# Optimization experiments

Measured on AMD Instinct MI355X. Metric: run time of the kernel, lower is better.

The kernel has to match this reference:

```python
import jax, jax.numpy as jnp
import numpy as np

EPS = 1e-6  # torch F.pairwise_distance default eps (added to diff before norm)


def setup_inputs() -> dict:
    key = jax.random.key(0)
    k1, k2 = jax.random.split(key)
    B, D, n = 4096, 1024, 64
    K = n * n
    x = jax.random.normal(k1, (B, D), dtype=jnp.float32)
    weight = jax.random.normal(k2, (D, K), dtype=jnp.float32)  # SOM codebook
    # locations = [(gx, gy) for gx in range(n) for gy in range(n)]
    gx, gy = jnp.meshgrid(jnp.arange(n), jnp.arange(n), indexing='ij')
    locations = jnp.stack([gx, gy], axis=-1).reshape(K, 2).astype(jnp.float32)
    return {"x": x, "weight": weight, "locations": locations}


def _pairwise_l2(x, weight):
    # torch: norm(x[:, :, None] - weight[None] + EPS, p=2, dim=1) -> [B, K]
    # Expanded algebraically to avoid the [B, D, K] intermediate:
    D = x.shape[1]
    x2 = jnp.sum(x * x, axis=1, keepdims=True)            # [B, 1]
    w2 = jnp.sum(weight * weight, axis=0, keepdims=True)  # [1, K]
    xw = x @ weight                                        # [B, K] GEMM
    sx = jnp.sum(x, axis=1, keepdims=True)                 # [B, 1]
    sw = jnp.sum(weight, axis=0, keepdims=True)            # [1, K]
    d2 = x2 - 2.0 * xw + w2 + 2.0 * EPS * (sx - sw) + D * EPS * EPS
    return jnp.sqrt(jnp.maximum(d2, 0.0))


def reference(x, weight, locations):
    B = x.shape[0]
    dists = _pairwise_l2(x, weight)                        # [B, K]
    losses = jnp.min(dists, axis=1, keepdims=True)         # [B, 1]
    bmu_indexes = jnp.argmin(dists, axis=1, keepdims=True)  # [B, 1] int
    bmu_locations = locations[bmu_indexes]                 # [B, 1, 2]
    loss = jnp.sum(losses) / B                             # scalar
    return bmu_locations, loss, bmu_indexes
```

## Files before the change

kernel.cpp:

```cpp
#include <hip/hip_runtime.h>

#define EPS 1e-6f

constexpr int Bn = 4096;
constexpr int Dn = 1024;
constexpr int Kn = 4096;

typedef __attribute__((ext_vector_type(4))) float f32x4;
typedef __attribute__((ext_vector_type(2))) long long ll2;

__device__ inline int pk_fp8_lo(float a, float b, int old) {
    return __builtin_amdgcn_cvt_pk_fp8_f32(a, b, old, false);
}
__device__ inline int pk_fp8_hi(float a, float b, int old) {
    return __builtin_amdgcn_cvt_pk_fp8_f32(a, b, old, true);
}

__device__ inline float packcand(float s, int k) {
    unsigned b = __float_as_uint(fmaxf(s, 0.5f));
    return __uint_as_float((b & 0xFFFFF000u) | (unsigned)k);
}

__global__ __launch_bounds__(256) void som_prep(
    const float* __restrict__ x, const float* __restrict__ w,
    unsigned char* __restrict__ xf8, float* __restrict__ rrow,
    float* __restrict__ wtf, unsigned char* __restrict__ wf8,
    float* __restrict__ cpart) {
    __shared__ float t[64][65];
    __shared__ float cp[4][64];
    __shared__ float red[8];
    const int tid = threadIdx.x;
    const int bid = blockIdx.x;
    if (bid < 2048) {
        const int lane = tid & 63, wid = tid >> 6;
        size_t i = (size_t)bid * 256 + tid;
        const float4* p = (const float4*)x;
        float4 a = p[i * 2], b = p[i * 2 + 1];
        int lo = pk_fp8_lo(a.x, a.y, 0); lo = pk_fp8_hi(a.z, a.w, lo);
        int hi = pk_fp8_lo(b.x, b.y, 0); hi = pk_fp8_hi(b.z, b.w, hi);
        ((int2*)xf8)[i] = make_int2(lo, hi);
        float s2 = a.x*a.x + a.y*a.y + a.z*a.z + a.w*a.w
                 + b.x*b.x + b.y*b.y + b.z*b.z + b.w*b.w;
        float s1 = a.x + a.y + a.z + a.w + b.x + b.y + b.z + b.w;
        #pragma unroll
        for (int off = 1; off < 64; off <<= 1) {
            s2 += __shfl_xor(s2, off);
            s1 += __shfl_xor(s1, off);
        }
        if (lane == 0) { red[wid] = s2; red[4 + wid] = s1; }
        __syncthreads();
        if (tid == 0)
            rrow[bid * 2] = (red[0] + red[1])
                + 2.f * EPS * (red[4] + red[5]) + (float)Dn * EPS * EPS;
        if (tid == 128)
            rrow[bid * 2 + 1] = (red[2] + red[3])
                + 2.f * EPS * (red[6] + red[7]) + (float)Dn * EPS * EPS;
    } else {
        const int tb = bid - 2048;
        const int kb = tb & 63, db = tb >> 6;
        const int k0 = kb * 64, d0 = db * 64;
        const int tx = tid & 63, ty = tid >> 6;
        #pragma unroll
        for (int i = 0; i < 16; ++i) {
            int d = i * 4 + ty;
            t[d][tx] = w[(size_t)(d0 + d) * Kn + k0 + tx];
        }
        __syncthreads();
        #pragma unroll
        for (int i = 0; i < 16; ++i) {
            int kr = i * 4 + ty;
            float v = t[tx][kr];
            wtf[(size_t)(k0 + kr) * Dn + d0 + tx] = v;
            wf8[(size_t)(k0 + kr) * Dn + d0 + tx] =
                (unsigned char)(pk_fp8_lo(v, v, 0) & 0xFF);
        }
        float cs = 0.f;
        #pragma unroll
        for (int j = 0; j < 16; ++j) {
            float v = t[ty * 16 + j][tx];
            cs = fmaf(v, v - 2.f * EPS, cs);
        }
        cp[ty][tx] = cs;
        __syncthreads();
        if (ty == 0)
            cpart[(size_t)db * Kn + k0 + tx] = cp[0][tx] + cp[1][tx] + cp[2][tx] + cp[3][tx];
    }
}

__global__ __launch_bounds__(256, 3) void som_gemm_fp8(
    const unsigned char* __restrict__ xf8, const unsigned char* __restrict__ wf8,
    const float* __restrict__ cpart, float* __restrict__ pval) {
    __shared__ __align__(16) unsigned char As[128 * 144];
    __shared__ __align__(16) unsigned char Bs[128 * 144];
    const int tid = threadIdx.x;
    const int lane = tid & 63;
    const int wid = tid >> 6;
    const int wm = wid >> 1, wn = wid & 1;
    const int f = blockIdx.x;
    const int xcd = f & 7;
    const int ib = f >> 3;
    const int rb = xcd * 4 + (ib & 3);
    const int cb = ib >> 2;
    const int rowBase = rb * 128, colBase = cb * 128;

    int offA[4];
    const unsigned char* gsrcA[4];
    const unsigned char* gsrcB[4];
    #pragma unroll
    for (int i = 0; i < 4; ++i) {
        int g = i * 256 + tid;
        int r = g >> 3, s = g & 7;
        offA[i] = r * 144 + (2 * (s & 1)) * 32 + (s >> 1) * 8;
        gsrcA[i] = xf8 + (size_t)(rowBase + r) * Dn + s * 16;
        gsrcB[i] = wf8 + (size_t)(colBase + r) * Dn + s * 16;
    }

    f32x4 acc[4][4] = {};
    ll2 ra[4], rbv[4];
    #pragma unroll
    for (int i = 0; i < 4; ++i) {
        ra[i]  = *(const ll2*)(gsrcA[i]);
        rbv[i] = *(const ll2*)(gsrcB[i]);
    }

    const int mrA = (wm * 64 + (lane & 15)) * 144;
    const int nrB = (wn * 64 + (lane & 15)) * 144;
    const int qoff = (lane >> 4) * 32;

    for (int it = 0; it < 8; ++it) {
        #pragma unroll
        for (int i = 0; i < 4; ++i) {
            *(long long*)&As[offA[i]]      = ra[i][0];
            *(long long*)&As[offA[i] + 32] = ra[i][1];
            *(long long*)&Bs[offA[i]]      = rbv[i][0];
            *(long long*)&Bs[offA[i] + 32] = rbv[i][1];
        }
        __syncthreads();
        if (it < 7) {
            int d0 = (it + 1) * 128;
            #pragma unroll
            for (int i = 0; i < 4; ++i) {
                ra[i]  = *(const ll2*)(gsrcA[i] + d0);
                rbv[i] = *(const ll2*)(gsrcB[i] + d0);
            }
        }
        #pragma unroll
        for (int kk2 = 0; kk2 < 2; ++kk2) {
            ll2 a2[4], b2[4];
            #pragma unroll
            for (int i = 0; i < 4; ++i) {
                a2[i] = *(const ll2*)&As[mrA + i * 16 * 144 + qoff + kk2 * 16];
                b2[i] = *(const ll2*)&Bs[nrB + i * 16 * 144 + qoff + kk2 * 16];
            }
            #pragma unroll
            for (int i = 0; i < 4; ++i)
                #pragma unroll
                for (int j = 0; j < 4; ++j) {
                    acc[i][j] = __builtin_amdgcn_mfma_f32_16x16x32_fp8_fp8(
                        a2[i][0], b2[j][0], acc[i][j], 0, 0, 0);
                    acc[i][j] = __builtin_amdgcn_mfma_f32_16x16x32_fp8_fp8(
                        a2[i][1], b2[j][1], acc[i][j], 0, 0, 0);
                }
        }
        __syncthreads();
    }

    const int cn = lane & 15, q = lane >> 4;
    const int nbase = colBase + wn * 64;
    float cv[4];
    #pragma unroll
    for (int j = 0; j < 4; ++j) {
        float s = 0.f;
        #pragma unroll
        for (int db = 0; db < 16; ++db)
            s += cpart[(size_t)db * Kn + nbase + j * 16 + cn];
        cv[j] = s;
    }
    #pragma unroll
    for (int i = 0; i < 4; ++i) {
        #pragma unroll
        for (int rg = 0; rg < 4; ++rg) {
            float p1 = 3.4e38f, p2 = 3.4e38f;
            #pragma unroll
            for (int j = 0; j < 4; ++j) {
                float p = packcand(fmaf(-2.f, acc[i][j][rg], cv[j]),
                                   nbase + j * 16 + cn);
                float lo = fminf(p1, p), hi = fmaxf(p1, p);
                p1 = lo; p2 = fminf(p2, hi);
            }
            #pragma unroll
            for (int off = 1; off < 16; off <<= 1) {
                float o1 = __shfl_xor(p1, off);
                float o2 = __shfl_xor(p2, off);
                float lo = fminf(p1, o1), hi = fmaxf(p1, o1);
                p1 = lo; p2 = fminf(hi, fminf(p2, o2));
            }
            if (cn == 0) {
                int mrow = rowBase + wm * 64 + i * 16 + q * 4 + rg;
                size_t e = (size_t)mrow * 128 + cb * 4 + wn * 2;
                pval[e] = p1; pval[e + 1] = p2;
            }
        }
    }
}

__global__ __launch_bounds__(256) void som_finalize(
    const float* __restrict__ x, const float* __restrict__ wtf,
    const float* __restrict__ cpart, const float* __restrict__ loc,
    const float* __restrict__ pval, const float* __restrict__ rrow,
    float* __restrict__ dist, float* __restrict__ out) {
    const int lane = threadIdx.x & 63;
    const int row = blockIdx.x * 4 + (threadIdx.x >> 6);

    const float4* xr = (const float4*)(x + (size_t)row * Dn);
    float4 xv[4];
    #pragma unroll
    for (int j = 0; j < 4; ++j) xv[j] = xr[lane * 4 + j];
    const float rrv = rrow[row];

    float v0 = pval[(size_t)row * 128 + lane];
    float v1 = pval[(size_t)row * 128 + 64 + lane];
    float g = fminf(v0, v1);
    #pragma unroll
    for (int off = 1; off < 64; off <<= 1) g = fminf(g, __shfl_xor(g, off));
    const float thr = g + 30.0f;
    unsigned long long m0 = __ballot(v0 <= thr);
    unsigned long long m1 = __ballot(v1 <= thr);

    float bestd2 = 3.4e38f; int bestk = 0x7fffffff;
    #pragma unroll
    for (int slot = 0; slot < 2; ++slot) {
        unsigned long long m = slot ? m1 : m0;
        float vs = slot ? v1 : v0;
        while (m) {
            int src = __builtin_ctzll(m); m &= m - 1;
            int k = ((int)__float_as_uint(__shfl(vs, src))) & 0xFFF;
            const float4* wr = (const float4*)(wtf + (size_t)k * Dn);
            float dt = 0.f;
            #pragma unroll
            for (int j = 0; j < 4; ++j) {
                float4 wv = wr[lane * 4 + j];
                dt += xv[j].x * wv.x + xv[j].y * wv.y + xv[j].z * wv.z + xv[j].w * wv.w;
            }
            #pragma unroll
            for (int off = 1; off < 64; off <<= 1) dt += __shfl_xor(dt, off);
            float ck = 0.f;
            #pragma unroll
            for (int db = 0; db < 16; ++db) ck += cpart[(size_t)db * Kn + k];
            float d2 = rrv + ck - 2.f * dt;
            if (d2 < bestd2 || (d2 == bestd2 && k < bestk)) { bestd2 = d2; bestk = k; }
        }
    }
    if (lane == 0) {
        out[2 * row]     = loc[2 * bestk];
        out[2 * row + 1] = loc[2 * bestk + 1];
        out[8193 + row]  = (float)bestk;
        dist[row]        = sqrtf(fmaxf(bestd2, 0.f));
    }
}

__global__ __launch_bounds__(256) void som_loss(const float* __restrict__ dist,
                                                float* __restrict__ out) {
    __shared__ float red[4];
    const int tid = threadIdx.x;
    const int lane = tid & 63, wid = tid >> 6;
    const float4* p = (const float4*)dist;
    float s = 0.f;
    #pragma unroll
    for (int j = 0; j < 4; ++j) {
        float4 v = p[tid + j * 256];
        s += v.x + v.y + v.z + v.w;
    }
    #pragma unroll
    for (int off = 1; off < 64; off <<= 1) s += __shfl_xor(s, off);
    if (lane == 0) red[wid] = s;
    __syncthreads();
    if (tid == 0)
        out[8192] = (red[0] + red[1] + red[2] + red[3]) * (1.0f / (float)Bn);
}

extern "C" void kernel_launch(void* const* d_in, const int* in_sizes, int n_in,
                              void* d_out, int out_size, void* d_ws, size_t ws_size,
                              hipStream_t stream) {
    const float* x   = (const float*)d_in[0];
    const float* w   = (const float*)d_in[1];
    const float* loc = (const float*)d_in[2];
    float* out = (float*)d_out;

    float* rrow = (float*)d_ws;
    float* wtf  = rrow + Bn;
    unsigned char* wf8 = (unsigned char*)(wtf + (size_t)Kn * Dn);
    unsigned char* xf8 = wf8 + (size_t)Kn * Dn;
    float* pval = (float*)(xf8 + (size_t)Bn * Dn);
    float* cpart = pval + (size_t)Bn * 128;
    float* dist  = cpart + 16 * Kn;

    som_prep<<<3072, 256, 0, stream>>>(x, w, xf8, rrow, wtf, wf8, cpart);
    som_gemm_fp8<<<1024, 256, 0, stream>>>(xf8, wf8, cpart, pval);
    som_finalize<<<Bn / 4, 256, 0, stream>>>(x, wtf, cpart, loc, pval, rrow, dist, out);
    som_loss<<<1, 256, 0, stream>>>(dist, out);
}
```

Measured before the change: 141.0 us.

## Switch screening GEMM from FP8 to INT8 MFMA and fuse loss into finalize

Replaces the FP8 quantization and 16x16x32 fp8 MFMA screening GEMM with symmetric int8 quantization (scale 31.75) and the 16x16x64 i8 MFMA issued through inline asm, using 16-byte LDS stores and loads. The candidate threshold in finalize is tightened from 30 to 20, which cuts exact-distance rechecks but risks missing the true argmin if the quantization error is larger than the margin. The separate single-block loss kernel is removed. Instead the last finalize block, found with an atomic ticket counter, does the reduction, saving one launch at the cost of atomics.

```diff
diff --git a/kernel.cpp b/kernel.cpp
--- a/kernel.cpp
+++ b/kernel.cpp
@@ -6,14 +6,15 @@
 constexpr int Dn = 1024;
 constexpr int Kn = 4096;
 
+constexpr float QS = 31.75f;
+constexpr float NEG2INV = -2.0f / (QS * QS);
+
 typedef __attribute__((ext_vector_type(4))) float f32x4;
+typedef __attribute__((ext_vector_type(4))) int i32x4;
 typedef __attribute__((ext_vector_type(2))) long long ll2;
 
-__device__ inline int pk_fp8_lo(float a, float b, int old) {
-    return __builtin_amdgcn_cvt_pk_fp8_f32(a, b, old, false);
-}
-__device__ inline int pk_fp8_hi(float a, float b, int old) {
-    return __builtin_amdgcn_cvt_pk_fp8_f32(a, b, old, true);
+__device__ inline int q8(float v) {
+    return (int)rintf(fminf(fmaxf(v * QS, -127.f), 127.f));
 }
 
 __device__ inline float packcand(float s, int k) {
@@ -23,22 +24,25 @@
 
 __global__ __launch_bounds__(256) void som_prep(
     const float* __restrict__ x, const float* __restrict__ w,
-    unsigned char* __restrict__ xf8, float* __restrict__ rrow,
-    float* __restrict__ wtf, unsigned char* __restrict__ wf8,
-    float* __restrict__ cpart) {
+    signed char* __restrict__ xq, float* __restrict__ rrow,
+    float* __restrict__ wtf, signed char* __restrict__ wq,
+    float* __restrict__ cpart, unsigned* __restrict__ ticket) {
     __shared__ float t[64][65];
     __shared__ float cp[4][64];
     __shared__ float red[8];
     const int tid = threadIdx.x;
     const int bid = blockIdx.x;
+    if (bid == 0 && tid == 32) *ticket = 0u;
     if (bid < 2048) {
         const int lane = tid & 63, wid = tid >> 6;
         size_t i = (size_t)bid * 256 + tid;
         const float4* p = (const float4*)x;
         float4 a = p[i * 2], b = p[i * 2 + 1];
-        int lo = pk_fp8_lo(a.x, a.y, 0); lo = pk_fp8_hi(a.z, a.w, lo);
-        int hi = pk_fp8_lo(b.x, b.y, 0); hi = pk_fp8_hi(b.z, b.w, hi);
-        ((int2*)xf8)[i] = make_int2(lo, hi);
+        int lo = (q8(a.x) & 255) | ((q8(a.y) & 255) << 8)
+               | ((q8(a.z) & 255) << 16) | (q8(a.w) << 24);
+        int hi = (q8(b.x) & 255) | ((q8(b.y) & 255) << 8)
+               | ((q8(b.z) & 255) << 16) | (q8(b.w) << 24);
+        ((int2*)xq)[i] = make_int2(lo, hi);
         float s2 = a.x*a.x + a.y*a.y + a.z*a.z + a.w*a.w
                  + b.x*b.x + b.y*b.y + b.z*b.z + b.w*b.w;
         float s1 = a.x + a.y + a.z + a.w + b.x + b.y + b.z + b.w;
@@ -71,8 +75,7 @@
             int kr = i * 4 + ty;
             float v = t[tx][kr];
             wtf[(size_t)(k0 + kr) * Dn + d0 + tx] = v;
-            wf8[(size_t)(k0 + kr) * Dn + d0 + tx] =
-                (unsigned char)(pk_fp8_lo(v, v, 0) & 0xFF);
+            wq[(size_t)(k0 + kr) * Dn + d0 + tx] = (signed char)q8(v);
         }
         float cs = 0.f;
         #pragma unroll
@@ -87,11 +90,11 @@
     }
 }
 
-__global__ __launch_bounds__(256, 3) void som_gemm_fp8(
-    const unsigned char* __restrict__ xf8, const unsigned char* __restrict__ wf8,
+__global__ __launch_bounds__(256, 3) void som_gemm_i8(
+    const signed char* __restrict__ xq, const signed char* __restrict__ wq,
     const float* __restrict__ cpart, float* __restrict__ pval) {
-    __shared__ __align__(16) unsigned char As[128 * 144];
-    __shared__ __align__(16) unsigned char Bs[128 * 144];
+    __shared__ __align__(16) signed char As[128 * 144];
+    __shared__ __align__(16) signed char Bs[128 * 144];
     const int tid = threadIdx.x;
     const int lane = tid & 63;
     const int wid = tid >> 6;
@@ -104,18 +107,18 @@
     const int rowBase = rb * 128, colBase = cb * 128;
 
     int offA[4];
-    const unsigned char* gsrcA[4];
-    const unsigned char* gsrcB[4];
+    const signed char* gsrcA[4];
+    const signed char* gsrcB[4];
     #pragma unroll
     for (int i = 0; i < 4; ++i) {
         int g = i * 256 + tid;
         int r = g >> 3, s = g & 7;
-        offA[i] = r * 144 + (2 * (s & 1)) * 32 + (s >> 1) * 8;
-        gsrcA[i] = xf8 + (size_t)(rowBase + r) * Dn + s * 16;
-        gsrcB[i] = wf8 + (size_t)(colBase + r) * Dn + s * 16;
-    }
-
-    f32x4 acc[4][4] = {};
+        offA[i] = r * 144 + (s & 3) * 32 + (s >> 2) * 16;
+        gsrcA[i] = xq + (size_t)(rowBase + r) * Dn + s * 16;
+        gsrcB[i] = wq + (size_t)(colBase + r) * Dn + s * 16;
+    }
+
+    i32x4 acc[4][4] = {};
     ll2 ra[4], rbv[4];
     #pragma unroll
     for (int i = 0; i < 4; ++i) {
@@ -130,10 +133,8 @@
     for (int it = 0; it < 8; ++it) {
         #pragma unroll
         for (int i = 0; i < 4; ++i) {
-            *(long long*)&As[offA[i]]      = ra[i][0];
-            *(long long*)&As[offA[i] + 32] = ra[i][1];
-            *(long long*)&Bs[offA[i]]      = rbv[i][0];
-            *(long long*)&Bs[offA[i] + 32] = rbv[i][1];
+            *(ll2*)&As[offA[i]] = ra[i];
+            *(ll2*)&Bs[offA[i]] = rbv[i];
         }
         __syncthreads();
         if (it < 7) {
@@ -144,23 +145,23 @@
                 rbv[i] = *(const ll2*)(gsrcB[i] + d0);
             }
         }
-        #pragma unroll
-        for (int kk2 = 0; kk2 < 2; ++kk2) {
-            ll2 a2[4], b2[4];
-            #pragma unroll
-            for (int i = 0; i < 4; ++i) {
-                a2[i] = *(const ll2*)&As[mrA + i * 16 * 144 + qoff + kk2 * 16];
-                b2[i] = *(const ll2*)&Bs[nrB + i * 16 * 144 + qoff + kk2 * 16];
-            }
-            #pragma unroll
-            for (int i = 0; i < 4; ++i)
-                #pragma unroll
-                for (int j = 0; j < 4; ++j) {
-                    acc[i][j] = __builtin_amdgcn_mfma_f32_16x16x32_fp8_fp8(
-                        a2[i][0], b2[j][0], acc[i][j], 0, 0, 0);
-                    acc[i][j] = __builtin_amdgcn_mfma_f32_16x16x32_fp8_fp8(
-                        a2[i][1], b2[j][1], acc[i][j], 0, 0, 0);
-                }
+        i32x4 bfr[4][2];
+        #pragma unroll
+        for (int j = 0; j < 4; ++j) {
+            bfr[j][0] = *(const i32x4*)&Bs[nrB + j * 16 * 144 + qoff];
+            bfr[j][1] = *(const i32x4*)&Bs[nrB + j * 16 * 144 + qoff + 16];
+        }
+        #pragma unroll
+        for (int i = 0; i < 4; ++i) {
+            i32x4 a0 = *(const i32x4*)&As[mrA + i * 16 * 144 + qoff];
+            i32x4 a1 = *(const i32x4*)&As[mrA + i * 16 * 144 + qoff + 16];
+            #pragma unroll
+            for (int j = 0; j < 4; ++j) {
+                asm("v_mfma_i32_16x16x64_i8 %0, %1, %2, %0"
+                    : "+a"(acc[i][j]) : "v"(a0), "v"(bfr[j][0]));
+                asm("v_mfma_i32_16x16x64_i8 %0, %1, %2, %0"
+                    : "+a"(acc[i][j]) : "v"(a1), "v"(bfr[j][1]));
+            }
         }
         __syncthreads();
     }
@@ -183,7 +184,7 @@
             float p1 = 3.4e38f, p2 = 3.4e38f;
             #pragma unroll
             for (int j = 0; j < 4; ++j) {
-                float p = packcand(fmaf(-2.f, acc[i][j][rg], cv[j]),
+                float p = packcand(fmaf(NEG2INV, (float)acc[i][j][rg], cv[j]),
                                    nbase + j * 16 + cn);
                 float lo = fminf(p1, p), hi = fmaxf(p1, p);
                 p1 = lo; p2 = fminf(p2, hi);
@@ -208,9 +209,13 @@
     const float* __restrict__ x, const float* __restrict__ wtf,
     const float* __restrict__ cpart, const float* __restrict__ loc,
     const float* __restrict__ pval, const float* __restrict__ rrow,
-    float* __restrict__ dist, float* __restrict__ out) {
-    const int lane = threadIdx.x & 63;
-    const int row = blockIdx.x * 4 + (threadIdx.x >> 6);
+    float* __restrict__ dist, float* __restrict__ out,
+    unsigned* __restrict__ ticket) {
+    __shared__ float red2[4];
+    __shared__ int finflag;
+    const int tid = threadIdx.x;
+    const int lane = tid & 63;
+    const int row = blockIdx.x * 4 + (tid >> 6);
 
     const float4* xr = (const float4*)(x + (size_t)row * Dn);
     float4 xv[4];
@@ -223,7 +228,7 @@
     float g = fminf(v0, v1);
     #pragma unroll
     for (int off = 1; off < 64; off <<= 1) g = fminf(g, __shfl_xor(g, off));
-    const float thr = g + 30.0f;
+    const float thr = g + 20.0f;
     unsigned long long m0 = __ballot(v0 <= thr);
     unsigned long long m1 = __ballot(v1 <= thr);
 
@@ -255,28 +260,35 @@
         out[2 * row]     = loc[2 * bestk];
         out[2 * row + 1] = loc[2 * bestk + 1];
         out[8193 + row]  = (float)bestk;
-        dist[row]        = sqrtf(fmaxf(bestd2, 0.f));
-    }
-}
-
-__global__ __launch_bounds__(256) void som_loss(const float* __restrict__ dist,
-                                                float* __restrict__ out) {
-    __shared__ float red[4];
-    const int tid = threadIdx.x;
-    const int lane = tid & 63, wid = tid >> 6;
-    const float4* p = (const float4*)dist;
-    float s = 0.f;
-    #pragma unroll
-    for (int j = 0; j < 4; ++j) {
-        float4 v = p[tid + j * 256];
-        s += v.x + v.y + v.z + v.w;
-    }
-    #pragma unroll
-    for (int off = 1; off < 64; off <<= 1) s += __shfl_xor(s, off);
-    if (lane == 0) red[wid] = s;
+        __hip_atomic_store(&dist[row], sqrtf(fmaxf(bestd2, 0.f)),
+                           __ATOMIC_RELAXED, __HIP_MEMORY_SCOPE_AGENT);
+    }
     __syncthreads();
-    if (tid == 0)
-        out[8192] = (red[0] + red[1] + red[2] + red[3]) * (1.0f / (float)Bn);
+    if (tid == 0) {
+        unsigned t = __hip_atomic_fetch_add(ticket, 1u, __ATOMIC_ACQ_REL,
+                                            __HIP_MEMORY_SCOPE_AGENT);
+        finflag = (t == (unsigned)gridDim.x - 1u);
+    }
+    __syncthreads();
+    if (finflag) {
+        const int wid = tid >> 6;
+        float s = 0.f;
+        #pragma unroll
+        for (int j = 0; j < 4; ++j) {
+            int base = (tid + j * 256) * 4;
+            float d0 = __hip_atomic_load(&dist[base + 0], __ATOMIC_RELAXED, __HIP_MEMORY_SCOPE_AGENT);
+            float d1 = __hip_atomic_load(&dist[base + 1], __ATOMIC_RELAXED, __HIP_MEMORY_SCOPE_AGENT);
+            float d2 = __hip_atomic_load(&dist[base + 2], __ATOMIC_RELAXED, __HIP_MEMORY_SCOPE_AGENT);
+            float d3 = __hip_atomic_load(&dist[base + 3], __ATOMIC_RELAXED, __HIP_MEMORY_SCOPE_AGENT);
+            s += ((d0 + d1) + d2) + d3;
+        }
+        #pragma unroll
+        for (int off = 1; off < 64; off <<= 1) s += __shfl_xor(s, off);
+        if (lane == 0) red2[wid] = s;
+        __syncthreads();
+        if (tid == 0)
+            out[8192] = (red2[0] + red2[1] + red2[2] + red2[3]) * (1.0f / (float)Bn);
+    }
 }
 
 extern "C" void kernel_launch(void* const* d_in, const int* in_sizes, int n_in,
@@ -289,14 +301,14 @@
 
     float* rrow = (float*)d_ws;
     float* wtf  = rrow + Bn;
-    unsigned char* wf8 = (unsigned char*)(wtf + (size_t)Kn * Dn);
-    unsigned char* xf8 = wf8 + (size_t)Kn * Dn;
-    float* pval = (float*)(xf8 + (size_t)Bn * Dn);
+    signed char* wq = (signed char*)(wtf + (size_t)Kn * Dn);
+    signed char* xq = wq + (size_t)Kn * Dn;
+    float* pval = (float*)(xq + (size_t)Bn * Dn);
     float* cpart = pval + (size_t)Bn * 128;
     float* dist  = cpart + 16 * Kn;
-
-    som_prep<<<3072, 256, 0, stream>>>(x, w, xf8, rrow, wtf, wf8, cpart);
-    som_gemm_fp8<<<1024, 256, 0, stream>>>(xf8, wf8, cpart, pval);
-    som_finalize<<<Bn / 4, 256, 0, stream>>>(x, wtf, cpart, loc, pval, rrow, dist, out);
-    som_loss<<<1, 256, 0, stream>>>(dist, out);
-}
+    unsigned* ticket = (unsigned*)(dist + Bn);
+
+    som_prep<<<3072, 256, 0, stream>>>(x, w, xq, rrow, wtf, wq, cpart, ticket);
+    som_gemm_i8<<<1024, 256, 0, stream>>>(xq, wq, cpart, pval);
+    som_finalize<<<Bn / 4, 256, 0, stream>>>(x, wtf, cpart, loc, pval, rrow, dist, out, ticket);
+}
```

Measured after the change: 148.4 us. 5.3% more time.

## Fuse loss reduction into finalize via ticket counter and batch candidate rescoring

Applied to the files above, without the earlier changes.

Drops the separate single-block loss kernel: the last finalize block, picked by an atomic ticket counter reset in the prep kernel, sums the per-row distances. Candidate indices are compacted into a shared-memory list and rescored two at a time, with the 16 cpart partials loaded in parallel across lanes and folded into the same shuffle reduction. This removes a launch and the serial per-candidate shuffle/cpart loop, at the cost of atomics and a dependency on ticket reset ordering.

```diff
diff --git a/kernel.cpp b/kernel.cpp
--- a/kernel.cpp
+++ b/kernel.cpp
@@ -25,12 +25,13 @@
     const float* __restrict__ x, const float* __restrict__ w,
     unsigned char* __restrict__ xf8, float* __restrict__ rrow,
     float* __restrict__ wtf, unsigned char* __restrict__ wf8,
-    float* __restrict__ cpart) {
+    float* __restrict__ cpart, unsigned* __restrict__ ticket) {
     __shared__ float t[64][65];
     __shared__ float cp[4][64];
     __shared__ float red[8];
     const int tid = threadIdx.x;
     const int bid = blockIdx.x;
+    if (bid == 0 && tid == 32) *ticket = 0u;
     if (bid < 2048) {
         const int lane = tid & 63, wid = tid >> 6;
         size_t i = (size_t)bid * 256 + tid;
@@ -208,9 +209,14 @@
     const float* __restrict__ x, const float* __restrict__ wtf,
     const float* __restrict__ cpart, const float* __restrict__ loc,
     const float* __restrict__ pval, const float* __restrict__ rrow,
-    float* __restrict__ dist, float* __restrict__ out) {
-    const int lane = threadIdx.x & 63;
-    const int row = blockIdx.x * 4 + (threadIdx.x >> 6);
+    float* __restrict__ dist, float* __restrict__ out,
+    unsigned* __restrict__ ticket) {
+    __shared__ unsigned short lists[4][128];
+    __shared__ float red2[4];
+    __shared__ int finflag;
+    const int tid = threadIdx.x;
+    const int wv = tid >> 6, lane = tid & 63;
+    const int row = blockIdx.x * 4 + wv;
 
     const float4* xr = (const float4*)(x + (size_t)row * Dn);
     float4 xv[4];
@@ -224,59 +230,80 @@
     #pragma unroll
     for (int off = 1; off < 64; off <<= 1) g = fminf(g, __shfl_xor(g, off));
     const float thr = g + 30.0f;
-    unsigned long long m0 = __ballot(v0 <= thr);
-    unsigned long long m1 = __ballot(v1 <= thr);
+    const unsigned long long m0 = __ballot(v0 <= thr);
+    const unsigned long long m1 = __ballot(v1 <= thr);
+    const int c0 = __popcll(m0);
+    const int cnt = c0 + __popcll(m1);
+    const unsigned long long below = (1ull << lane) - 1;
+    if (v0 <= thr)
+        lists[wv][__popcll(m0 & below)] =
+            (unsigned short)(__float_as_uint(v0) & 0xFFF);
+    if (v1 <= thr)
+        lists[wv][c0 + __popcll(m1 & below)] =
+            (unsigned short)(__float_as_uint(v1) & 0xFFF);
 
     float bestd2 = 3.4e38f; int bestk = 0x7fffffff;
-    #pragma unroll
-    for (int slot = 0; slot < 2; ++slot) {
-        unsigned long long m = slot ? m1 : m0;
-        float vs = slot ? v1 : v0;
-        while (m) {
-            int src = __builtin_ctzll(m); m &= m - 1;
-            int k = ((int)__float_as_uint(__shfl(vs, src))) & 0xFFF;
-            const float4* wr = (const float4*)(wtf + (size_t)k * Dn);
-            float dt = 0.f;
-            #pragma unroll
-            for (int j = 0; j < 4; ++j) {
-                float4 wv = wr[lane * 4 + j];
-                dt += xv[j].x * wv.x + xv[j].y * wv.y + xv[j].z * wv.z + xv[j].w * wv.w;
-            }
-            #pragma unroll
-            for (int off = 1; off < 64; off <<= 1) dt += __shfl_xor(dt, off);
-            float ck = 0.f;
-            #pragma unroll
-            for (int db = 0; db < 16; ++db) ck += cpart[(size_t)db * Kn + k];
-            float d2 = rrv + ck - 2.f * dt;
-            if (d2 < bestd2 || (d2 == bestd2 && k < bestk)) { bestd2 = d2; bestk = k; }
+    for (int i = 0; i < cnt; i += 2) {
+        const int ka = lists[wv][i];
+        const int kb = lists[wv][(i + 1 < cnt) ? i + 1 : i];
+        const float4* wra = (const float4*)(wtf + (size_t)ka * Dn);
+        const float4* wrb = (const float4*)(wtf + (size_t)kb * Dn);
+        float pa = (lane < 16) ? cpart[(size_t)lane * Kn + ka] : 0.f;
+        float pb = (lane < 16) ? cpart[(size_t)lane * Kn + kb] : 0.f;
+        float da = 0.f, db = 0.f;
+        #pragma unroll
+        for (int j = 0; j < 4; ++j) {
+            float4 wa = wra[lane * 4 + j];
+            float4 wb = wrb[lane * 4 + j];
+            da += xv[j].x * wa.x + xv[j].y * wa.y + xv[j].z * wa.z + xv[j].w * wa.w;
+            db += xv[j].x * wb.x + xv[j].y * wb.y + xv[j].z * wb.z + xv[j].w * wb.w;
+        }
+        pa -= 2.f * da;
+        pb -= 2.f * db;
+        #pragma unroll
+        for (int off = 1; off < 64; off <<= 1) {
+            pa += __shfl_xor(pa, off);
+            pb += __shfl_xor(pb, off);
+        }
+        const float d2a = rrv + pa, d2b = rrv + pb;
+        if (d2a < bestd2 || (d2a == bestd2 && ka < bestk)) { bestd2 = d2a; bestk = ka; }
+        if (i + 1 < cnt && (d2b < bestd2 || (d2b == bestd2 && kb < bestk))) {
+            bestd2 = d2b; bestk = kb;
         }
     }
     if (lane == 0) {
         out[2 * row]     = loc[2 * bestk];
         out[2 * row + 1] = loc[2 * bestk + 1];
         out[8193 + row]  = (float)bestk;
-        dist[row]        = sqrtf(fmaxf(bestd2, 0.f));
-    }
-}
-
-__global__ __launch_bounds__(256) void som_loss(const float* __restrict__ dist,
-                                                float* __restrict__ out) {
-    __shared__ float red[4];
-    const int tid = threadIdx.x;
-    const int lane = tid & 63, wid = tid >> 6;
-    const float4* p = (const float4*)dist;
-    float s = 0.f;
-    #pragma unroll
-    for (int j = 0; j < 4; ++j) {
-        float4 v = p[tid + j * 256];
-        s += v.x + v.y + v.z + v.w;
-    }
-    #pragma unroll
-    for (int off = 1; off < 64; off <<= 1) s += __shfl_xor(s, off);
-    if (lane == 0) red[wid] = s;
+        __hip_atomic_store(&dist[row], sqrtf(fmaxf(bestd2, 0.f)),
+                           __ATOMIC_RELAXED, __HIP_MEMORY_SCOPE_AGENT);
+    }
     __syncthreads();
-    if (tid == 0)
-        out[8192] = (red[0] + red[1] + red[2] + red[3]) * (1.0f / (float)Bn);
+    if (tid == 0) {
+        unsigned t = __hip_atomic_fetch_add(ticket, 1u, __ATOMIC_ACQ_REL,
+                                            __HIP_MEMORY_SCOPE_AGENT);
+        finflag = (t == (unsigned)gridDim.x - 1u);
+    }
+    __syncthreads();
+    if (finflag) {
+        const int wid = tid >> 6;
+        float s = 0.f;
+        #pragma unroll
+        for (int j = 0; j < 4; ++j) {
+            int base = (tid + j * 256) * 4;
+            float d0 = __hip_atomic_load(&dist[base + 0], __ATOMIC_RELAXED, __HIP_MEMORY_SCOPE_AGENT);
+            float d1 = __hip_atomic_load(&dist[base + 1], __ATOMIC_RELAXED, __HIP_MEMORY_SCOPE_AGENT);
+            float d2 = __hip_atomic_load(&dist[base + 2], __ATOMIC_RELAXED, __HIP_MEMORY_SCOPE_AGENT);
+            float d3 = __hip_atomic_load(&dist[base + 3], __ATOMIC_RELAXED, __HIP_MEMORY_SCOPE_AGENT);
+            s += ((d0 + d1) + d2) + d3;
+        }
+        #pragma unroll
+        for (int off = 1; off < 64; off <<= 1) s += __shfl_xor(s, off);
+        if (lane == 0) red2[wid] = s;
+        __syncthreads();
+        if (tid == 0)
+            out[8192] = (red2[0] + red2[1] + red2[2] + red2[3]) * (1.0f / (float)Bn);
+    }
 }
 
 extern "C" void kernel_launch(void* const* d_in, const int* in_sizes, int n_in,
@@ -294,9 +321,9 @@
     float* pval = (float*)(xf8 + (size_t)Bn * Dn);
     float* cpart = pval + (size_t)Bn * 128;
     float* dist  = cpart + 16 * Kn;
-
-    som_prep<<<3072, 256, 0, stream>>>(x, w, xf8, rrow, wtf, wf8, cpart);
+    unsigned* ticket = (unsigned*)(dist + Bn);
+
+    som_prep<<<3072, 256, 0, stream>>>(x, w, xf8, rrow, wtf, wf8, cpart, ticket);
     som_gemm_fp8<<<1024, 256, 0, stream>>>(xf8, wf8, cpart, pval);
-    som_finalize<<<Bn / 4, 256, 0, stream>>>(x, wtf, cpart, loc, pval, rrow, dist, out);
-    som_loss<<<1, 256, 0, stream>>>(dist, out);
-}
+    som_finalize<<<Bn / 4, 256, 0, stream>>>(x, wtf, cpart, loc, pval, rrow, dist, out, ticket);
+}
```

Result: slower. 160.3 us (+13.7%).
